# Optimization experiments

Hardware: AMD Instinct MI355X
Metric: run time of the kernel (lower is better)

The kernel has to match this reference:

```python
import jax, jax.numpy as jnp
import numpy as np

B, S, K, H = 512, 128, 4, 128  # batch, seq_len, interest_num, hidden_size
ROUTING_TIMES = 3
EPS = 1e-9


def setup_inputs() -> dict:
    key = jax.random.key(0)
    k1, k2 = jax.random.split(key)
    item_eb = jax.random.normal(k1, (B, S, H), dtype=jnp.float32)
    mask = jnp.ones((B, S), dtype=jnp.float32)
    # learned bilinear map parameter (bilinear_type == 2)
    w = jax.random.normal(k2, (1, S, K * H, H), dtype=jnp.float32) * 0.02
    return {"item_eb": item_eb, "mask": mask, "w": w}


def _squash(cap):
    # cap: [B, K, 1, H]
    n = jnp.sum(cap * cap, axis=-1, keepdims=True)
    return (n / (1.0 + n) / jnp.sqrt(n + EPS)) * cap


def reference(item_eb, mask, w):
    # bilinear_type==2: sum(w[:, :S] * item_eb[:, :, None, :], axis=3)
    # expressed as an einsum to avoid the [B,S,K*H,H] intermediate
    item_eb_hat = jnp.einsum('bsh,sdh->bsd', item_eb, w[0])          # [B, S, K*H]
    item_eb_hat = item_eb_hat.reshape(B, S, K, H).transpose(0, 2, 1, 3)  # [B, K, S, H]
    hat_iter = jax.lax.stop_gradient(item_eb_hat)  # stop_grad=True

    atten_mask = jnp.broadcast_to(mask[:, None, :], (B, K, S))
    capsule_weight = jnp.zeros((B, K, S), dtype=item_eb.dtype)  # bilinear_type > 0

    interest_capsule = None
    for i in range(ROUTING_TIMES):
        # torch F.softmax with implicit dim on a 3D tensor -> dim=0 (legacy)
        sw = jax.nn.softmax(capsule_weight, axis=0)
        sw = jnp.where(atten_mask == 0, 0.0, sw)[:, :, None, :]  # [B, K, 1, S]
        src = hat_iter if i < 2 else item_eb_hat
        interest_capsule = _squash(jnp.matmul(sw, src))  # [B, K, 1, H]
        if i < 2:
            delta = jnp.matmul(hat_iter, interest_capsule.transpose(0, 1, 3, 2))  # [B,K,S,1]
            capsule_weight = capsule_weight + delta.reshape(B, K, S)

    return interest_capsule.reshape(B, K, H)
```

## Files before the change

kernel.cpp:

```cpp
#include <hip/hip_runtime.h>
#include <math.h>

#define BB 512
#define SS 128
#define KK 4
#define HH 128
#define DD 512

typedef __attribute__((ext_vector_type(8))) short bf16x8;
typedef __attribute__((ext_vector_type(4))) float f32x4;

__device__ __forceinline__ unsigned short f2bf(float f) {
  unsigned u = __float_as_uint(f);
  unsigned r = u + 0x7fffu + ((u >> 16) & 1u);
  return (unsigned short)(r >> 16);
}
__device__ __forceinline__ float bfhi(unsigned u) { return __uint_as_float(u & 0xffff0000u); }
__device__ __forceinline__ float bflo(unsigned u) { return __uint_as_float(u << 16); }

__global__ __launch_bounds__(256) void prep_k(
    const float* __restrict__ item, const float* __restrict__ w,
    unsigned short* __restrict__ item_t, unsigned short* __restrict__ w_bf)
{
  const int blk = blockIdx.x, t = threadIdx.x;
  if (blk < 8192) {
    const int rid = blk * 8 + (t >> 5);
    const int b = rid >> 7, s = rid & 127;
    const int c = t & 31;
    float4 v = ((const float4*)(item + (size_t)rid * HH))[c];
    ushort4 o;
    o.x = f2bf(v.x); o.y = f2bf(v.y); o.z = f2bf(v.z); o.w = f2bf(v.w);
    ((ushort4*)(item_t + ((size_t)s * BB + b) * HH))[c] = o;
  } else {
    size_t base = (size_t)(blk - 8192) * 2048 + t;
    const float4* src = (const float4*)w;
    ushort4* dst = (ushort4*)w_bf;
    #pragma unroll
    for (int j = 0; j < 8; j++) {
      float4 v = src[base + 256 * j];
      ushort4 o;
      o.x = f2bf(v.x); o.y = f2bf(v.y); o.z = f2bf(v.z); o.w = f2bf(v.w);
      dst[base + 256 * j] = o;
    }
  }
}

__global__ __launch_bounds__(256) void einsum_mfma(
    const unsigned short* __restrict__ At,
    const unsigned short* __restrict__ W,
    unsigned short* __restrict__ hat)
{
  __shared__ unsigned short Al[128 * 64];
  __shared__ unsigned short Wl[128 * 64];
  const int s  = blockIdx.x;
  const int b0 = (blockIdx.y & 3) * 128;
  const int dt = blockIdx.y >> 2;
  const int d0 = dt * 128;
  const int t  = threadIdx.x;
  const int lane = t & 63, wv = t >> 6;
  const int qm = wv & 1, qn = wv >> 1;
  const int n16 = lane & 15, kq = lane >> 4;
  const int sr = t >> 3, sc = t & 7;

  const unsigned short* Abase = At + ((size_t)s * BB + b0) * HH;
  const unsigned short* Wbase = W + ((size_t)s * DD + d0) * HH;

  f32x4 acc[4][4] = {};
  for (int ks = 0; ks < 128; ks += 64) {
    #pragma unroll
    for (int j = 0; j < 4; j++) {
      const int r = sr + 32 * j;
      uint4 va = *(const uint4*)(Abase + (size_t)r * HH + ks + sc * 8);
      uint4 vw = *(const uint4*)(Wbase + (size_t)r * HH + ks + sc * 8);
      const int goff = ((sc + r) & 7) * 8;
      *(uint4*)&Al[r * 64 + goff] = va;
      *(uint4*)&Wl[r * 64 + goff] = vw;
    }
    __syncthreads();
    #pragma unroll
    for (int kk = 0; kk < 2; kk++) {
      bf16x8 af[4], bfr[4];
      #pragma unroll
      for (int i = 0; i < 4; i++) {
        const int ra = qm * 64 + i * 16 + n16;
        const int rb = qn * 64 + i * 16 + n16;
        af[i]  = *(const bf16x8*)&Wl[ra * 64 + ((kk * 4 + kq + ra) & 7) * 8];
        bfr[i] = *(const bf16x8*)&Al[rb * 64 + ((kk * 4 + kq + rb) & 7) * 8];
      }
      #pragma unroll
      for (int i = 0; i < 4; i++)
        #pragma unroll
        for (int j = 0; j < 4; j++)
          acc[i][j] = __builtin_amdgcn_mfma_f32_16x16x32_bf16(af[i], bfr[j], acc[i][j], 0, 0, 0);
    }
    __syncthreads();
  }

  #pragma unroll
  for (int j = 0; j < 4; j++) {
    const int b = b0 + qn * 64 + j * 16 + n16;
    unsigned short* orow = hat + (((size_t)b * KK + dt) * SS + s) * HH;
    #pragma unroll
    for (int i = 0; i < 4; i++) {
      const int h = qm * 64 + i * 16 + kq * 4;
      ushort4 o;
      o.x = f2bf(acc[i][j][0]); o.y = f2bf(acc[i][j][1]);
      o.z = f2bf(acc[i][j][2]); o.w = f2bf(acc[i][j][3]);
      *(ushort4*)(orow + h) = o;
    }
  }
}

__global__ __launch_bounds__(256) void softmax_k(
    const float* __restrict__ cw, const float* __restrict__ mask,
    float* __restrict__ sw)
{
  __shared__ float rbuf[4];
  const int s = blockIdx.x, k = blockIdx.y, t = threadIdx.x;
  const size_t base = ((size_t)k * SS + s) * BB;
  float v0 = cw[base + t], v1 = cw[base + 256 + t];
  float m = fmaxf(v0, v1);
  #pragma unroll
  for (int o = 32; o; o >>= 1) m = fmaxf(m, __shfl_xor(m, o));
  if ((t & 63) == 0) rbuf[t >> 6] = m;
  __syncthreads();
  m = fmaxf(fmaxf(rbuf[0], rbuf[1]), fmaxf(rbuf[2], rbuf[3]));
  float e0 = expf(v0 - m), e1 = expf(v1 - m);
  float ssum = e0 + e1;
  #pragma unroll
  for (int o = 32; o; o >>= 1) ssum += __shfl_xor(ssum, o);
  __syncthreads();
  if ((t & 63) == 0) rbuf[t >> 6] = ssum;
  __syncthreads();
  float inv = 1.f / (rbuf[0] + rbuf[1] + rbuf[2] + rbuf[3]);
  float m0 = mask[(size_t)t * SS + s];
  float m1 = mask[(size_t)(t + 256) * SS + s];
  sw[base + t]       = (m0 == 0.f) ? 0.f : e0 * inv;
  sw[base + 256 + t] = (m1 == 0.f) ? 0.f : e1 * inv;
}

__global__ __launch_bounds__(256) void routing_k(
    const unsigned short* __restrict__ hat, const float* __restrict__ mask,
    const float* __restrict__ sw_in, float* __restrict__ cw,
    float* __restrict__ out, int mode)
{
  __shared__ unsigned short hat_l[128 * 136];
  __shared__ float sw_l[128];
  __shared__ float4 red4[8][32];
  __shared__ float4 cq4[32];
  const int b = blockIdx.x, k = blockIdx.y, t = threadIdx.x;

  if (t < 128) {
    sw_l[t] = (mode == 0)
      ? ((mask[(size_t)b * SS + t] == 0.f) ? 0.f : (1.f / 512.f))
      : sw_in[((size_t)k * SS + t) * BB + b];
  }
  const uint4* hp = (const uint4*)(hat + ((size_t)b * KK + k) * SS * HH);
  #pragma unroll
  for (int j = 0; j < 8; j++) {
    const int f = t + 256 * j;
    const int s = f >> 4, c = f & 15;
    *(uint4*)&hat_l[s * 136 + c * 8] = hp[f];
  }
  __syncthreads();

  {
    const int h4 = t & 31, sg = t >> 5;
    float4 a = make_float4(0.f, 0.f, 0.f, 0.f);
    #pragma unroll 4
    for (int i = 0; i < 16; i++) {
      const int s = sg * 16 + i;
      uint2 v = *(const uint2*)&hat_l[s * 136 + h4 * 4];
      float wv = sw_l[s];
      a.x = fmaf(wv, bflo(v.x), a.x);
      a.y = fmaf(wv, bfhi(v.x), a.y);
      a.z = fmaf(wv, bflo(v.y), a.z);
      a.w = fmaf(wv, bfhi(v.y), a.w);
    }
    red4[sg][h4] = a;
  }
  __syncthreads();

  if (t < 32) {
    float4 cap = red4[0][t];
    #pragma unroll
    for (int sg = 1; sg < 8; sg++) {
      float4 r = red4[sg][t];
      cap.x += r.x; cap.y += r.y; cap.z += r.z; cap.w += r.w;
    }
    float sq = cap.x * cap.x + cap.y * cap.y + cap.z * cap.z + cap.w * cap.w;
    #pragma unroll
    for (int o = 16; o; o >>= 1) sq += __shfl_xor(sq, o);
    const float n = sq;
    const float fac = n / (1.f + n) / sqrtf(n + 1e-9f);
    cap.x *= fac; cap.y *= fac; cap.z *= fac; cap.w *= fac;
    cq4[t] = cap;
    if (mode == 2)
      ((float4*)(out + ((size_t)b * KK + k) * HH))[t] = cap;
  }
  __syncthreads();

  if (mode < 2) {
    const int s = t >> 1, hh = t & 1;
    const uint4* row = (const uint4*)&hat_l[s * 136 + hh * 64];
    float d = 0.f;
    #pragma unroll
    for (int j = 0; j < 8; j++) {
      uint4 v = row[j];
      float4 qa = cq4[hh * 16 + 2 * j];
      float4 qb = cq4[hh * 16 + 2 * j + 1];
      d += bflo(v.x) * qa.x + bfhi(v.x) * qa.y
         + bflo(v.y) * qa.z + bfhi(v.y) * qa.w
         + bflo(v.z) * qb.x + bfhi(v.z) * qb.y
         + bflo(v.w) * qb.z + bfhi(v.w) * qb.w;
    }
    d += __shfl_xor(d, 1);
    if (hh == 0) {
      float* p = cw + ((size_t)k * SS + s) * BB + b;
      if (mode == 0) *p = d; else *p += d;
    }
  }
}

extern "C" void kernel_launch(void* const* d_in, const int* in_sizes, int n_in,
                              void* d_out, int out_size, void* d_ws, size_t ws_size,
                              hipStream_t stream) {
  const float* item_eb = (const float*)d_in[0];
  const float* mask    = (const float*)d_in[1];
  const float* w       = (const float*)d_in[2];
  float* out = (float*)d_out;

  char* ws = (char*)d_ws;
  unsigned short* hat_bf  = (unsigned short*)ws;
  unsigned short* item_t  = (unsigned short*)(ws + 67108864);
  unsigned short* w_bf    = (unsigned short*)(ws + 83886080);
  float* cw  = (float*)(ws + 100663296);
  float* swb = (float*)(ws + 101711872);

  prep_k<<<dim3(9216), 256, 0, stream>>>(item_eb, w, item_t, w_bf);
  einsum_mfma<<<dim3(128, 16), 256, 0, stream>>>(item_t, w_bf, hat_bf);

  routing_k<<<dim3(BB, KK), 256, 0, stream>>>(hat_bf, mask, nullptr, cw, out, 0);
  softmax_k<<<dim3(SS, KK), 256, 0, stream>>>(cw, mask, swb);
  routing_k<<<dim3(BB, KK), 256, 0, stream>>>(hat_bf, mask, swb, cw, out, 1);
  softmax_k<<<dim3(SS, KK), 256, 0, stream>>>(cw, mask, swb);
  routing_k<<<dim3(BB, KK), 256, 0, stream>>>(hat_bf, mask, swb, cw, out, 2);
}
```

Before: 184.6 us.

## Fuse bf16 conversion into einsum and async-load swizzled hat tiles in routing

Drops the separate prep kernel and has the MFMA einsum read fp32 item and w directly, converting to bf16 as it fills shared memory. It also writes the hat output in an XOR-swizzled layout, so routing_k can copy each slab straight into LDS with global_load_lds async copies, without padding and without bank conflicts. This removes one launch and the round trip through global memory for the bf16 copies. In exchange, the einsum loads twice the bytes per tile and must strided-gather item across s, which may cost bandwidth inside the GEMM.

```diff
diff --git a/kernel.cpp b/kernel.cpp
--- a/kernel.cpp
+++ b/kernel.cpp
@@ -18,36 +18,15 @@
 __device__ __forceinline__ float bfhi(unsigned u) { return __uint_as_float(u & 0xffff0000u); }
 __device__ __forceinline__ float bflo(unsigned u) { return __uint_as_float(u << 16); }
 
-__global__ __launch_bounds__(256) void prep_k(
-    const float* __restrict__ item, const float* __restrict__ w,
-    unsigned short* __restrict__ item_t, unsigned short* __restrict__ w_bf)
-{
-  const int blk = blockIdx.x, t = threadIdx.x;
-  if (blk < 8192) {
-    const int rid = blk * 8 + (t >> 5);
-    const int b = rid >> 7, s = rid & 127;
-    const int c = t & 31;
-    float4 v = ((const float4*)(item + (size_t)rid * HH))[c];
-    ushort4 o;
-    o.x = f2bf(v.x); o.y = f2bf(v.y); o.z = f2bf(v.z); o.w = f2bf(v.w);
-    ((ushort4*)(item_t + ((size_t)s * BB + b) * HH))[c] = o;
-  } else {
-    size_t base = (size_t)(blk - 8192) * 2048 + t;
-    const float4* src = (const float4*)w;
-    ushort4* dst = (ushort4*)w_bf;
-    #pragma unroll
-    for (int j = 0; j < 8; j++) {
-      float4 v = src[base + 256 * j];
-      ushort4 o;
-      o.x = f2bf(v.x); o.y = f2bf(v.y); o.z = f2bf(v.z); o.w = f2bf(v.w);
-      dst[base + 256 * j] = o;
-    }
-  }
+__device__ __forceinline__ void async_cp16(const void* g, void* l) {
+  __builtin_amdgcn_global_load_lds(
+      (const __attribute__((address_space(1))) unsigned int*)g,
+      (__attribute__((address_space(3))) unsigned int*)l, 16, 0, 0);
 }
 
 __global__ __launch_bounds__(256) void einsum_mfma(
-    const unsigned short* __restrict__ At,
-    const unsigned short* __restrict__ W,
+    const float* __restrict__ item,
+    const float* __restrict__ w,
     unsigned short* __restrict__ hat)
 {
   __shared__ unsigned short Al[128 * 64];
@@ -60,21 +39,26 @@
   const int lane = t & 63, wv = t >> 6;
   const int qm = wv & 1, qn = wv >> 1;
   const int n16 = lane & 15, kq = lane >> 4;
-  const int sr = t >> 3, sc = t & 7;
-
-  const unsigned short* Abase = At + ((size_t)s * BB + b0) * HH;
-  const unsigned short* Wbase = W + ((size_t)s * DD + d0) * HH;
+  const int cj = t & 15, r0 = t >> 4;
+
+  const float* Abase = item + ((size_t)b0 * SS + s) * HH;
+  const float* Wbase = w + ((size_t)s * DD + d0) * HH;
 
   f32x4 acc[4][4] = {};
+  #pragma unroll
   for (int ks = 0; ks < 128; ks += 64) {
-    #pragma unroll
-    for (int j = 0; j < 4; j++) {
-      const int r = sr + 32 * j;
-      uint4 va = *(const uint4*)(Abase + (size_t)r * HH + ks + sc * 8);
-      uint4 vw = *(const uint4*)(Wbase + (size_t)r * HH + ks + sc * 8);
-      const int goff = ((sc + r) & 7) * 8;
-      *(uint4*)&Al[r * 64 + goff] = va;
-      *(uint4*)&Wl[r * 64 + goff] = vw;
+    if (ks) __syncthreads();
+    #pragma unroll
+    for (int j = 0; j < 8; j++) {
+      const int r = r0 + 16 * j;
+      float4 va = *(const float4*)(Abase + (size_t)r * (SS * HH) + ks + cj * 4);
+      float4 vw = *(const float4*)(Wbase + (size_t)r * HH + ks + cj * 4);
+      ushort4 oa, ow;
+      oa.x = f2bf(va.x); oa.y = f2bf(va.y); oa.z = f2bf(va.z); oa.w = f2bf(va.w);
+      ow.x = f2bf(vw.x); ow.y = f2bf(vw.y); ow.z = f2bf(vw.z); ow.w = f2bf(vw.w);
+      const int goff = (((cj >> 1) + r) & 7) * 8 + (cj & 1) * 4;
+      *(ushort4*)&Al[r * 64 + goff] = oa;
+      *(ushort4*)&Wl[r * 64 + goff] = ow;
     }
     __syncthreads();
     #pragma unroll
@@ -93,20 +77,20 @@
         for (int j = 0; j < 4; j++)
           acc[i][j] = __builtin_amdgcn_mfma_f32_16x16x32_bf16(af[i], bfr[j], acc[i][j], 0, 0, 0);
     }
-    __syncthreads();
-  }
-
+  }
+
+  const int sx = s & 15;
   #pragma unroll
   for (int j = 0; j < 4; j++) {
     const int b = b0 + qn * 64 + j * 16 + n16;
-    unsigned short* orow = hat + (((size_t)b * KK + dt) * SS + s) * HH;
+    char* orow = (char*)(hat + (((size_t)b * KK + dt) * SS + s) * HH);
     #pragma unroll
     for (int i = 0; i < 4; i++) {
       const int h = qm * 64 + i * 16 + kq * 4;
       ushort4 o;
       o.x = f2bf(acc[i][j][0]); o.y = f2bf(acc[i][j][1]);
       o.z = f2bf(acc[i][j][2]); o.w = f2bf(acc[i][j][3]);
-      *(ushort4*)(orow + h) = o;
+      *(ushort4*)(orow + ((((h >> 3) ^ sx) << 4) | ((h & 4) << 1))) = o;
     }
   }
 }
@@ -144,38 +128,40 @@
     const float* __restrict__ sw_in, float* __restrict__ cw,
     float* __restrict__ out, int mode)
 {
-  __shared__ unsigned short hat_l[128 * 136];
+  __shared__ unsigned short hat_l[128 * 128];
   __shared__ float sw_l[128];
   __shared__ float4 red4[8][32];
   __shared__ float4 cq4[32];
   const int b = blockIdx.x, k = blockIdx.y, t = threadIdx.x;
+  const int wv = t >> 6;
+
+  const char* slab = (const char*)(hat + ((size_t)b * KK + k) * SS * HH);
+  #pragma unroll
+  for (int j = 0; j < 8; j++)
+    async_cp16(slab + j * 4096 + t * 16,
+               (char*)hat_l + j * 4096 + wv * 1024);
 
   if (t < 128) {
     sw_l[t] = (mode == 0)
       ? ((mask[(size_t)b * SS + t] == 0.f) ? 0.f : (1.f / 512.f))
       : sw_in[((size_t)k * SS + t) * BB + b];
   }
-  const uint4* hp = (const uint4*)(hat + ((size_t)b * KK + k) * SS * HH);
-  #pragma unroll
-  for (int j = 0; j < 8; j++) {
-    const int f = t + 256 * j;
-    const int s = f >> 4, c = f & 15;
-    *(uint4*)&hat_l[s * 136 + c * 8] = hp[f];
-  }
   __syncthreads();
 
   {
     const int h4 = t & 31, sg = t >> 5;
+    const char* base = (const char*)hat_l;
     float4 a = make_float4(0.f, 0.f, 0.f, 0.f);
     #pragma unroll 4
     for (int i = 0; i < 16; i++) {
       const int s = sg * 16 + i;
-      uint2 v = *(const uint2*)&hat_l[s * 136 + h4 * 4];
-      float wv = sw_l[s];
-      a.x = fmaf(wv, bflo(v.x), a.x);
-      a.y = fmaf(wv, bfhi(v.x), a.y);
-      a.z = fmaf(wv, bflo(v.y), a.z);
-      a.w = fmaf(wv, bfhi(v.y), a.w);
+      uint2 v = *(const uint2*)(base + s * 256 +
+                 ((((h4 >> 1) ^ (s & 15)) << 4) | ((h4 & 1) << 3)));
+      float wv2 = sw_l[s];
+      a.x = fmaf(wv2, bflo(v.x), a.x);
+      a.y = fmaf(wv2, bfhi(v.x), a.y);
+      a.z = fmaf(wv2, bflo(v.y), a.z);
+      a.w = fmaf(wv2, bfhi(v.y), a.w);
     }
     red4[sg][h4] = a;
   }
@@ -202,11 +188,12 @@
 
   if (mode < 2) {
     const int s = t >> 1, hh = t & 1;
-    const uint4* row = (const uint4*)&hat_l[s * 136 + hh * 64];
+    const char* rowp = (const char*)hat_l + s * 256;
+    const int sx = s & 15;
     float d = 0.f;
     #pragma unroll
     for (int j = 0; j < 8; j++) {
-      uint4 v = row[j];
+      uint4 v = *(const uint4*)(rowp + (((hh * 8 + j) ^ sx) << 4));
       float4 qa = cq4[hh * 16 + 2 * j];
       float4 qb = cq4[hh * 16 + 2 * j + 1];
       d += bflo(v.x) * qa.x + bfhi(v.x) * qa.y
@@ -231,14 +218,11 @@
   float* out = (float*)d_out;
 
   char* ws = (char*)d_ws;
-  unsigned short* hat_bf  = (unsigned short*)ws;
-  unsigned short* item_t  = (unsigned short*)(ws + 67108864);
-  unsigned short* w_bf    = (unsigned short*)(ws + 83886080);
-  float* cw  = (float*)(ws + 100663296);
-  float* swb = (float*)(ws + 101711872);
-
-  prep_k<<<dim3(9216), 256, 0, stream>>>(item_eb, w, item_t, w_bf);
-  einsum_mfma<<<dim3(128, 16), 256, 0, stream>>>(item_t, w_bf, hat_bf);
+  unsigned short* hat_bf = (unsigned short*)ws;
+  float* cw  = (float*)(ws + 67108864);
+  float* swb = (float*)(ws + 68157440);
+
+  einsum_mfma<<<dim3(128, 16), 256, 0, stream>>>(item_eb, w, hat_bf);
 
   routing_k<<<dim3(BB, KK), 256, 0, stream>>>(hat_bf, mask, nullptr, cw, out, 0);
   softmax_k<<<dim3(SS, KK), 256, 0, stream>>>(cw, mask, swb);
```

Result: faster. 174.4 us (-5.5%).
